# Kernel optimization log

Measured on AMD Instinct MI355X. Metric: run time of the kernel, lower is better.

The kernel has to match this reference:

```python
import jax, jax.numpy as jnp
import numpy as np

N = 50000       # num nodes
E = 800000      # num edges (before self loops)
D_IN = 128
D_H = 128
D_OUT = 40


def setup_inputs() -> dict:
    key = jax.random.key(0)
    ks = jax.random.split(key, 8)
    x = jax.random.normal(ks[0], (N, D_IN), dtype=jnp.float32)
    edge_index = jax.random.randint(ks[1], (2, E), 0, N, dtype=jnp.int32)
    # GCNConv weights (glorot-ish scale) and biases
    W1 = jax.random.normal(ks[2], (D_IN, D_H), dtype=jnp.float32) / np.sqrt(D_IN)
    b1 = jnp.zeros((D_H,), dtype=jnp.float32)
    W2 = jax.random.normal(ks[3], (D_H, D_H), dtype=jnp.float32) / np.sqrt(D_H)
    b2 = jnp.zeros((D_H,), dtype=jnp.float32)
    Wc = jax.random.normal(ks[4], (D_H, D_OUT), dtype=jnp.float32) / np.sqrt(D_H)
    bc = jnp.zeros((D_OUT,), dtype=jnp.float32)
    return {"x": x, "edge_index": edge_index, "W1": W1, "b1": b1,
            "W2": W2, "b2": b2, "Wc": Wc, "bc": bc}


def _gcn_conv(x, row, col, num_nodes, W, b):
    # PyG GCNConv: h = X @ W; out[c] += norm(r,c) * h[r]; out += b
    h = x @ W
    deg = jax.ops.segment_sum(jnp.ones(row.shape[0], h.dtype), col,
                              num_segments=num_nodes)
    dinv = jnp.where(deg > 0, jax.lax.rsqrt(deg), 0.0).astype(h.dtype)
    norm = dinv[row] * dinv[col]                      # [E+N]
    msg = h[row] * norm[:, None]                      # gather + scale
    agg = jax.ops.segment_sum(msg, col, num_segments=num_nodes)  # scatter-add
    return agg + b


def reference(x, edge_index, W1, b1, W2, b2, Wc, bc):
    # add self loops (GCNConv default add_self_loops=True)
    loops = jnp.arange(N, dtype=edge_index.dtype)
    row = jnp.concatenate([edge_index[0], loops])
    col = jnp.concatenate([edge_index[1], loops])
    h = jax.nn.relu(_gcn_conv(x, row, col, N, W1, b1))
    h = jax.nn.relu(_gcn_conv(h, row, col, N, W2, b2))
    g = jnp.mean(h, axis=0)                           # mean pool over nodes
    return g @ Wc + bc                                # [D_OUT]
```

## Files before the change

### kernel.cpp

```cpp
#include <hip/hip_runtime.h>
#include <hip/hip_fp16.h>


typedef _Float16 half8 __attribute__((ext_vector_type(8)));
typedef float f32x4 __attribute__((ext_vector_type(4)));
typedef float f32x2 __attribute__((ext_vector_type(2)));

constexpr int N = 50000;
constexpr int E = 800000;
constexpr int D = 128;
constexpr int DOUT = 40;
constexpr int CAP = 64;
constexpr int HB = 128;
constexpr int EPB = E / HB;
constexpr int HWRD = 12500;
constexpr int GM = (N + 127) / 128;
constexpr int NW = N / 4;
constexpr int GF = 3 * GM;

__global__ __launch_bounds__(1024) void k_hist(const int* __restrict__ col,
                                               unsigned char* __restrict__ hist,
                                               unsigned char* __restrict__ rank,
                                               const float* __restrict__ W1,
                                               const float* __restrict__ W2,
                                               __half* __restrict__ T1,
                                               __half* __restrict__ T2) {
    __shared__ unsigned int h[HWRD];
    int b = blockIdx.x, t = threadIdx.x;
    if (b >= HB) {
        int o = (b - HB) * 1024 + t;
        const float* W = (o < 16384) ? W1 : W2;
        __half* T = (o < 16384) ? T1 : T2;
        int oo = o & 16383;
        int n = oo >> 7, k = oo & 127;
        T[oo] = (__half)W[k * 128 + n];
        return;
    }
    for (int i = t; i < HWRD; i += 1024) h[i] = 0;
    __syncthreads();
    int e0 = b * EPB;
    for (int e = e0 + t; e < e0 + EPB; e += 1024) {
        int c = col[e];
        unsigned int old = atomicAdd(&h[c >> 2], 1u << ((c & 3) * 8));
        rank[e] = (unsigned char)((old >> ((c & 3) * 8)) & 0xff);
    }
    __syncthreads();
    unsigned int* out = (unsigned int*)(hist + (size_t)b * 50000);
    for (int i = t; i < HWRD; i += 1024) out[i] = h[i];
}

__global__ __launch_bounds__(256) void k_colscan(unsigned char* __restrict__ hist,
                                                 int* __restrict__ deg,
                                                 float* __restrict__ dinv) {
    __shared__ unsigned int part[4][64];
    unsigned int* hw = (unsigned int*)hist;
    int c4 = blockIdx.x * 64 + (threadIdx.x & 63);
    int qq = threadIdx.x >> 6;
    bool ok = c4 < HWRD;
    unsigned int v[32];
    unsigned int s = 0;
    if (ok) {
#pragma unroll
        for (int i = 0; i < 32; ++i) v[i] = hw[(size_t)(qq * 32 + i) * HWRD + c4];
#pragma unroll
        for (int i = 0; i < 32; ++i) s += v[i];
    }
    part[qq][threadIdx.x & 63] = s;
    __syncthreads();
    unsigned int base = 0;
    for (int k = 0; k < qq; ++k) base += part[k][threadIdx.x & 63];
    if (ok) {
        unsigned int run = base;
#pragma unroll
        for (int i = 0; i < 32; ++i) {
            hw[(size_t)(qq * 32 + i) * HWRD + c4] = run;
            run += v[i];
        }
        if (qq == 3) {
#pragma unroll
            for (int j = 0; j < 4; ++j) {
                int dg = (run >> (8 * j)) & 0xff;
                deg[4 * c4 + j] = dg;
                dinv[4 * c4 + j] = rsqrtf((float)(dg + 1));
            }
        }
    }
}

__device__ __forceinline__ unsigned char f8enc(float v) {
    return (unsigned char)(__builtin_amdgcn_cvt_pk_fp8_f32(v, v, 0, false) & 0xff);
}
__device__ __forceinline__ void add8f8(f32x2* a, uint2 u) {
    a[0] += __builtin_amdgcn_cvt_pk_f32_fp8(u.x, false);
    a[1] += __builtin_amdgcn_cvt_pk_f32_fp8(u.x, true);
    a[2] += __builtin_amdgcn_cvt_pk_f32_fp8(u.y, false);
    a[3] += __builtin_amdgcn_cvt_pk_f32_fp8(u.y, true);
}

__device__ __forceinline__ half8 ldA(const float* rowp, int koff) {
    float4 u0 = *(const float4*)(rowp + koff);
    float4 u1 = *(const float4*)(rowp + koff + 4);
    half8 r;
    r[0] = (_Float16)u0.x; r[1] = (_Float16)u0.y;
    r[2] = (_Float16)u0.z; r[3] = (_Float16)u0.w;
    r[4] = (_Float16)u1.x; r[5] = (_Float16)u1.y;
    r[6] = (_Float16)u1.z; r[7] = (_Float16)u1.w;
    return r;
}
__device__ __forceinline__ half8 ldA(const unsigned char* rowp, int koff) {
    uint2 u = *(const uint2*)(rowp + koff);
    f32x2 f0 = __builtin_amdgcn_cvt_pk_f32_fp8(u.x, false);
    f32x2 f1 = __builtin_amdgcn_cvt_pk_f32_fp8(u.x, true);
    f32x2 f2 = __builtin_amdgcn_cvt_pk_f32_fp8(u.y, false);
    f32x2 f3 = __builtin_amdgcn_cvt_pk_f32_fp8(u.y, true);
    half8 r;
    r[0] = (_Float16)f0[0]; r[1] = (_Float16)f0[1];
    r[2] = (_Float16)f1[0]; r[3] = (_Float16)f1[1];
    r[4] = (_Float16)f2[0]; r[5] = (_Float16)f2[1];
    r[6] = (_Float16)f3[0]; r[7] = (_Float16)f3[1];
    return r;
}

template <typename TA>
__device__ __forceinline__ void mfma_gemm(const TA* __restrict__ A,
                                          const __half* __restrict__ Wt,
                                          const float* __restrict__ dinv,
                                          unsigned char* __restrict__ out8,
                                          int row0, int tid) {
    int wave = tid >> 6, lane = tid & 63;
    int quad = lane >> 4, c16 = lane & 15;
    int m0 = row0 + wave * 32;
    int ra = m0 + c16;      if (ra >= N) ra = 0;
    int rb = m0 + 16 + c16; if (rb >= N) rb = 0;
    const TA* pa = A + (size_t)ra * D;
    const TA* pb = A + (size_t)rb * D;

    f32x4 acc[2][8];
#pragma unroll
    for (int i = 0; i < 2; ++i)
#pragma unroll
        for (int j = 0; j < 8; ++j) acc[i][j] = (f32x4){0.f, 0.f, 0.f, 0.f};

#pragma unroll
    for (int kq = 0; kq < 4; ++kq) {
        int koff = kq * 32 + quad * 8;
        half8 a0 = ldA(pa, koff);
        half8 a1 = ldA(pb, koff);
#pragma unroll
        for (int nt = 0; nt < 8; ++nt) {
            half8 bf = *(const half8*)(Wt + (size_t)(nt * 16 + c16) * D + koff);
            acc[0][nt] = __builtin_amdgcn_mfma_f32_16x16x32_f16(a0, bf, acc[0][nt], 0, 0, 0);
            acc[1][nt] = __builtin_amdgcn_mfma_f32_16x16x32_f16(a1, bf, acc[1][nt], 0, 0, 0);
        }
    }

#pragma unroll
    for (int rt = 0; rt < 2; ++rt) {
        int mt = m0 + rt * 16;
#pragma unroll
        for (int i = 0; i < 4; ++i) {
            int grow = mt + quad * 4 + i;
            if (grow < N) {
                float s = dinv[grow];
                unsigned char* orow = out8 + (size_t)grow * D + c16;
#pragma unroll
                for (int nt = 0; nt < 8; ++nt)
                    orow[nt * 16] = f8enc(acc[rt][nt][i] * s);
            }
        }
    }
}

__global__ __launch_bounds__(256) void k_fuse(const int* __restrict__ ei,
                                              const unsigned char* __restrict__ hist,
                                              const unsigned char* __restrict__ rank,
                                              unsigned short* __restrict__ csr,
                                              const float* __restrict__ x,
                                              const __half* __restrict__ Wt1,
                                              const float* __restrict__ dinv,
                                              unsigned char* __restrict__ out8) {
    int b = blockIdx.x, m = b % 3;
    if (m < 2) {
        int sb = (b / 3) * 2 + m;
        int e0 = sb * 1024 + threadIdx.x * 4;
        if (e0 >= E) return;
        int4 rr = *(const int4*)(ei + e0);
        int4 cc = *(const int4*)(ei + E + e0);
        uchar4 kk = *(const uchar4*)(rank + e0);
        int rs[4] = {rr.x, rr.y, rr.z, rr.w};
        int cs[4] = {cc.x, cc.y, cc.z, cc.w};
        int ks[4] = {kk.x, kk.y, kk.z, kk.w};
#pragma unroll
        for (int i = 0; i < 4; ++i) {
            int e = e0 + i;
            int c = cs[i];
            int chunk = e / EPB;
            int slot = (int)hist[(size_t)chunk * 50000 + c] + ks[i];
            if (slot < CAP) csr[(c << 6) + slot] = (unsigned short)rs[i];
        }
        return;
    }
    mfma_gemm<float>(x, Wt1, dinv, out8, (b / 3) * 128, threadIdx.x);
}

__device__ __forceinline__ float agg_core(int c, int lane,
                                          const unsigned char* __restrict__ hs8,
                                          const int* __restrict__ deg,
                                          const unsigned short* __restrict__ csr,
                                          float* __restrict__ a0out) {
    int qw = lane >> 4;
    int q  = lane & 15;
    int dgRaw = deg[c];
    int dg = dgRaw < CAP ? dgRaw : CAP;
    float dc = rsqrtf((float)(dgRaw + 1));
    int e0 = c << 6;

    f32x2 a0[4], a1[4], a2[4], a3[4];
#pragma unroll
    for (int i = 0; i < 4; ++i) {
        a0[i] = (f32x2){0.f, 0.f}; a1[i] = (f32x2){0.f, 0.f};
        a2[i] = (f32x2){0.f, 0.f}; a3[i] = (f32x2){0.f, 0.f};
    }
    if (qw == 0)
        add8f8(a0, *(const uint2*)&hs8[((unsigned)c << 7) + q * 8]);

    int j = 0;
    for (; j + 16 <= dg; j += 16) {
        int r0 = csr[e0 + j + qw];
        int r1 = csr[e0 + j + 4 + qw];
        int r2 = csr[e0 + j + 8 + qw];
        int r3 = csr[e0 + j + 12 + qw];
        uint2 u0 = *(const uint2*)&hs8[((unsigned)r0 << 7) + q * 8];
        uint2 u1 = *(const uint2*)&hs8[((unsigned)r1 << 7) + q * 8];
        uint2 u2 = *(const uint2*)&hs8[((unsigned)r2 << 7) + q * 8];
        uint2 u3 = *(const uint2*)&hs8[((unsigned)r3 << 7) + q * 8];
        add8f8(a0, u0); add8f8(a1, u1); add8f8(a2, u2); add8f8(a3, u3);
    }
    if (j + 8 <= dg) {
        int r0 = csr[e0 + j + qw];
        int r1 = csr[e0 + j + 4 + qw];
        uint2 u0 = *(const uint2*)&hs8[((unsigned)r0 << 7) + q * 8];
        uint2 u1 = *(const uint2*)&hs8[((unsigned)r1 << 7) + q * 8];
        add8f8(a0, u0); add8f8(a1, u1);
        j += 8;
    }
    if (j + 4 <= dg) {
        int r0 = csr[e0 + j + qw];
        add8f8(a0, *(const uint2*)&hs8[((unsigned)r0 << 7) + q * 8]);
        j += 4;
    }
    int rem = dg - j;
    if (qw < rem) {
        int r0 = csr[e0 + j + qw];
        add8f8(a1, *(const uint2*)&hs8[((unsigned)r0 << 7) + q * 8]);
    }

#pragma unroll
    for (int i = 0; i < 4; ++i) { a0[i] += a1[i]; a2[i] += a3[i]; a0[i] += a2[i]; }
#pragma unroll
    for (int t = 0; t < 8; ++t) {
        float v = a0[t >> 1][t & 1];
        v += __shfl_xor(v, 16, 64);
        v += __shfl_xor(v, 32, 64);
        a0out[t] = v;
    }
    return dc;
}

__global__ __launch_bounds__(256) void k_agg1(const unsigned char* __restrict__ hs8,
                                              const int* __restrict__ deg,
                                              const unsigned short* __restrict__ csr,
                                              const float* __restrict__ bias,
                                              unsigned char* __restrict__ out8) {
    int wave = threadIdx.x >> 6;
    int lane = threadIdx.x & 63;
    int c = blockIdx.x * 4 + wave;
    float a0[8];
    float dc = agg_core(c, lane, hs8, deg, csr, a0);
    if ((lane >> 4) == 0) {
        int q = lane & 15;
        union { unsigned char b[8]; uint2 u; } p;
#pragma unroll
        for (int i = 0; i < 8; ++i)
            p.b[i] = f8enc(fmaxf(fmaf(dc, a0[i], bias[q * 8 + i]), 0.f));
        *(uint2*)&out8[((unsigned)c << 7) + q * 8] = p.u;
    }
}

__global__ __launch_bounds__(256) void k_gemm(const unsigned char* __restrict__ A,
                                              const __half* __restrict__ Wt,
                                              const float* __restrict__ dinv,
                                              unsigned char* __restrict__ out8) {
    mfma_gemm<unsigned char>(A, Wt, dinv, out8, blockIdx.x * 128, threadIdx.x);
}

__global__ __launch_bounds__(256) void k_agg2(const unsigned char* __restrict__ hs8,
                                              const int* __restrict__ deg,
                                              const unsigned short* __restrict__ csr,
                                              const float* __restrict__ bias,
                                              float* __restrict__ gpart) {
    __shared__ float gblk[4][128];
    int wave = threadIdx.x >> 6;
    int lane = threadIdx.x & 63;
    int c = blockIdx.x * 4 + wave;
    float a0[8];
    float dc = agg_core(c, lane, hs8, deg, csr, a0);
    if ((lane >> 4) == 0) {
        int q = lane & 15;
#pragma unroll
        for (int i = 0; i < 8; ++i)
            gblk[wave][q * 8 + i] = fmaxf(fmaf(dc, a0[i], bias[q * 8 + i]), 0.f);
    }
    __syncthreads();
    int t = threadIdx.x;
    if (t < 128)
        gpart[(size_t)blockIdx.x * 128 + t] =
            gblk[0][t] + gblk[1][t] + gblk[2][t] + gblk[3][t];
}

__global__ __launch_bounds__(256) void k_pool(const float* __restrict__ gpart,
                                              float* __restrict__ gpart2) {
    int d = threadIdx.x & 127;
    int half = threadIdx.x >> 7;
    int b = blockIdx.x;
    int per = (NW + 255) / 256;
    int r0 = b * per;
    int r1 = r0 + per;
    if (r1 > NW) r1 = NW;
    float acc = 0.f;
    for (int r = r0 + half; r < r1; r += 2)
        acc += gpart[(size_t)r * D + d];
    __shared__ float red[256];
    red[threadIdx.x] = acc;
    __syncthreads();
    if (half == 0) gpart2[(size_t)b * D + d] = red[d] + red[128 + d];
}

__global__ __launch_bounds__(512) void k_final(const float* __restrict__ gpart2,
                                               const float* __restrict__ Wc,
                                               const float* __restrict__ bc,
                                               float* __restrict__ out) {
    __shared__ float g[D];
    __shared__ float red[512];
    int t = threadIdx.x;
    int d = t & 127, grp = t >> 7;
    float s = 0.f;
#pragma unroll 4
    for (int w = grp * 64; w < grp * 64 + 64; ++w)
        s += gpart2[(size_t)w * D + d];
    red[t] = s;
    __syncthreads();
    if (grp == 0)
        g[d] = (red[d] + red[128 + d] + red[256 + d] + red[384 + d]) * (1.0f / (float)N);
    __syncthreads();
    if (t < DOUT) {
        float acc = bc[t];
        for (int dd = 0; dd < D; ++dd) acc = fmaf(g[dd], Wc[dd * DOUT + t], acc);
        out[t] = acc;
    }
}

extern "C" void kernel_launch(void* const* d_in, const int* in_sizes, int n_in,
                              void* d_out, int out_size, void* d_ws, size_t ws_size,
                              hipStream_t stream) {
    const float* x  = (const float*)d_in[0];
    const int*   ei = (const int*)d_in[1];
    const float* W1 = (const float*)d_in[2];
    const float* b1 = (const float*)d_in[3];
    const float* W2 = (const float*)d_in[4];
    const float* b2 = (const float*)d_in[5];
    const float* Wc = (const float*)d_in[6];
    const float* bc = (const float*)d_in[7];
    float* out = (float*)d_out;

    char* ws = (char*)d_ws;
    size_t off = 0;
    auto alloc = [&](size_t bytes) {
        void* p = ws + off;
        off += (bytes + 511) & ~(size_t)511;
        return p;
    };
    unsigned char*  hist   = (unsigned char*) alloc((size_t)HB * 50000);
    unsigned char*  rank   = (unsigned char*) alloc((size_t)E);
    int*            deg    = (int*)           alloc((size_t)N * 4);
    float*          dinv   = (float*)         alloc((size_t)N * 4);
    unsigned short* csr    = (unsigned short*)alloc((size_t)N * CAP * 2);
    unsigned char*  hs8    = (unsigned char*) alloc((size_t)N * D);
    unsigned char*  h18    = (unsigned char*) alloc((size_t)N * D);
    __half*         Wt1    = (__half*)        alloc((size_t)D * D * 2);
    __half*         Wt2    = (__half*)        alloc((size_t)D * D * 2);
    float*          gpart  = (float*)         alloc((size_t)NW * D * 4);
    float*          gpart2 = (float*)         alloc((size_t)256 * D * 4);
    (void)ws_size; (void)in_sizes; (void)n_in; (void)out_size;

    const int* col = ei + E;

    k_hist<<<HB + 32, 1024, 0, stream>>>(col, hist, rank, W1, W2, Wt1, Wt2);
    k_colscan<<<(HWRD + 63) / 64, 256, 0, stream>>>(hist, deg, dinv);
    k_fuse<<<GF, 256, 0, stream>>>(ei, hist, rank, csr, x, Wt1, dinv, hs8);

    k_agg1<<<NW, 256, 0, stream>>>(hs8, deg, csr, b1, h18);
    k_gemm<<<GM, 256, 0, stream>>>(h18, Wt2, dinv, hs8);
    k_agg2<<<NW, 256, 0, stream>>>(hs8, deg, csr, b2, gpart);
    k_pool<<<256, 256, 0, stream>>>(gpart, gpart2);
    k_final<<<1, 512, 0, stream>>>(gpart2, Wc, bc, out);
}
```

Baseline: 206.3 us.

## Widen aggregation gathers to 16-byte rows and halve histogram block count

The neighbor aggregation now gives each source row to 8 lanes, each loading 16 bytes, so one wave covers 8 neighbors per step. All 64 CSR slots are read up front, and the feature loads are issued under per-slot predicates before any accumulation. This replaces the old variable-length loop and its tail handling, aiming for more loads in flight and fewer loop branches, at the cost of more registers. The edge histogram also drops from 128 to 64 chunks, which halves the histogram traffic and the column-scan work but gives each histogram block more edges to process.

Result: slower. 213.4 us (+3.5%).

```diff
diff --git a/kernel.cpp b/kernel.cpp
--- a/kernel.cpp
+++ b/kernel.cpp
@@ -11,7 +11,7 @@
 constexpr int D = 128;
 constexpr int DOUT = 40;
 constexpr int CAP = 64;
-constexpr int HB = 128;
+constexpr int HB = 64;
 constexpr int EPB = E / HB;
 constexpr int HWRD = 12500;
 constexpr int GM = (N + 127) / 128;
@@ -57,13 +57,13 @@
     int c4 = blockIdx.x * 64 + (threadIdx.x & 63);
     int qq = threadIdx.x >> 6;
     bool ok = c4 < HWRD;
-    unsigned int v[32];
+    unsigned int v[16];
     unsigned int s = 0;
     if (ok) {
 #pragma unroll
-        for (int i = 0; i < 32; ++i) v[i] = hw[(size_t)(qq * 32 + i) * HWRD + c4];
-#pragma unroll
-        for (int i = 0; i < 32; ++i) s += v[i];
+        for (int i = 0; i < 16; ++i) v[i] = hw[(size_t)(qq * 16 + i) * HWRD + c4];
+#pragma unroll
+        for (int i = 0; i < 16; ++i) s += v[i];
     }
     part[qq][threadIdx.x & 63] = s;
     __syncthreads();
@@ -72,8 +72,8 @@
     if (ok) {
         unsigned int run = base;
 #pragma unroll
-        for (int i = 0; i < 32; ++i) {
-            hw[(size_t)(qq * 32 + i) * HWRD + c4] = run;
+        for (int i = 0; i < 16; ++i) {
+            hw[(size_t)(qq * 16 + i) * HWRD + c4] = run;
             run += v[i];
         }
         if (qq == 3) {
@@ -90,11 +90,15 @@
 __device__ __forceinline__ unsigned char f8enc(float v) {
     return (unsigned char)(__builtin_amdgcn_cvt_pk_fp8_f32(v, v, 0, false) & 0xff);
 }
-__device__ __forceinline__ void add8f8(f32x2* a, uint2 u) {
+__device__ __forceinline__ void add16f8(f32x2* a, uint4 u) {
     a[0] += __builtin_amdgcn_cvt_pk_f32_fp8(u.x, false);
     a[1] += __builtin_amdgcn_cvt_pk_f32_fp8(u.x, true);
     a[2] += __builtin_amdgcn_cvt_pk_f32_fp8(u.y, false);
     a[3] += __builtin_amdgcn_cvt_pk_f32_fp8(u.y, true);
+    a[4] += __builtin_amdgcn_cvt_pk_f32_fp8(u.z, false);
+    a[5] += __builtin_amdgcn_cvt_pk_f32_fp8(u.z, true);
+    a[6] += __builtin_amdgcn_cvt_pk_f32_fp8(u.w, false);
+    a[7] += __builtin_amdgcn_cvt_pk_f32_fp8(u.w, true);
 }
 
 __device__ __forceinline__ half8 ldA(const float* rowp, int koff) {
@@ -208,58 +212,40 @@
                                           const int* __restrict__ deg,
                                           const unsigned short* __restrict__ csr,
                                           float* __restrict__ a0out) {
-    int qw = lane >> 4;
-    int q  = lane & 15;
+    int qw = lane >> 3;
+    int q  = lane & 7;
     int dgRaw = deg[c];
     int dg = dgRaw < CAP ? dgRaw : CAP;
     float dc = rsqrtf((float)(dgRaw + 1));
     int e0 = c << 6;
-
-    f32x2 a0[4], a1[4], a2[4], a3[4];
-#pragma unroll
-    for (int i = 0; i < 4; ++i) {
-        a0[i] = (f32x2){0.f, 0.f}; a1[i] = (f32x2){0.f, 0.f};
-        a2[i] = (f32x2){0.f, 0.f}; a3[i] = (f32x2){0.f, 0.f};
-    }
-    if (qw == 0)
-        add8f8(a0, *(const uint2*)&hs8[((unsigned)c << 7) + q * 8]);
-
-    int j = 0;
-    for (; j + 16 <= dg; j += 16) {
-        int r0 = csr[e0 + j + qw];
-        int r1 = csr[e0 + j + 4 + qw];
-        int r2 = csr[e0 + j + 8 + qw];
-        int r3 = csr[e0 + j + 12 + qw];
-        uint2 u0 = *(const uint2*)&hs8[((unsigned)r0 << 7) + q * 8];
-        uint2 u1 = *(const uint2*)&hs8[((unsigned)r1 << 7) + q * 8];
-        uint2 u2 = *(const uint2*)&hs8[((unsigned)r2 << 7) + q * 8];
-        uint2 u3 = *(const uint2*)&hs8[((unsigned)r3 << 7) + q * 8];
-        add8f8(a0, u0); add8f8(a1, u1); add8f8(a2, u2); add8f8(a3, u3);
-    }
-    if (j + 8 <= dg) {
-        int r0 = csr[e0 + j + qw];
-        int r1 = csr[e0 + j + 4 + qw];
-        uint2 u0 = *(const uint2*)&hs8[((unsigned)r0 << 7) + q * 8];
-        uint2 u1 = *(const uint2*)&hs8[((unsigned)r1 << 7) + q * 8];
-        add8f8(a0, u0); add8f8(a1, u1);
-        j += 8;
-    }
-    if (j + 4 <= dg) {
-        int r0 = csr[e0 + j + qw];
-        add8f8(a0, *(const uint2*)&hs8[((unsigned)r0 << 7) + q * 8]);
-        j += 4;
-    }
-    int rem = dg - j;
-    if (qw < rem) {
-        int r0 = csr[e0 + j + qw];
-        add8f8(a1, *(const uint2*)&hs8[((unsigned)r0 << 7) + q * 8]);
-    }
-
-#pragma unroll
-    for (int i = 0; i < 4; ++i) { a0[i] += a1[i]; a2[i] += a3[i]; a0[i] += a2[i]; }
-#pragma unroll
-    for (int t = 0; t < 8; ++t) {
-        float v = a0[t >> 1][t & 1];
+    int boff = q * 16;
+
+    int r[8];
+#pragma unroll
+    for (int b = 0; b < 8; ++b) r[b] = csr[e0 + b * 8 + qw];
+
+    uint4 us;
+    bool selfv = (qw == 0);
+    if (selfv) us = *(const uint4*)&hs8[((unsigned)c << 7) + boff];
+
+    uint4 u[8];
+#pragma unroll
+    for (int b = 0; b < 8; ++b)
+        if (b * 8 + qw < dg)
+            u[b] = *(const uint4*)&hs8[((unsigned)r[b] << 7) + boff];
+
+    f32x2 acc[8];
+#pragma unroll
+    for (int i = 0; i < 8; ++i) acc[i] = (f32x2){0.f, 0.f};
+    if (selfv) add16f8(acc, us);
+#pragma unroll
+    for (int b = 0; b < 8; ++b)
+        if (b * 8 + qw < dg) add16f8(acc, u[b]);
+
+#pragma unroll
+    for (int t = 0; t < 16; ++t) {
+        float v = acc[t >> 1][t & 1];
+        v += __shfl_xor(v, 8, 64);
         v += __shfl_xor(v, 16, 64);
         v += __shfl_xor(v, 32, 64);
         a0out[t] = v;
@@ -275,15 +261,15 @@
     int wave = threadIdx.x >> 6;
     int lane = threadIdx.x & 63;
     int c = blockIdx.x * 4 + wave;
-    float a0[8];
+    float a0[16];
     float dc = agg_core(c, lane, hs8, deg, csr, a0);
-    if ((lane >> 4) == 0) {
-        int q = lane & 15;
-        union { unsigned char b[8]; uint2 u; } p;
-#pragma unroll
-        for (int i = 0; i < 8; ++i)
-            p.b[i] = f8enc(fmaxf(fmaf(dc, a0[i], bias[q * 8 + i]), 0.f));
-        *(uint2*)&out8[((unsigned)c << 7) + q * 8] = p.u;
+    if (lane < 8) {
+        int q = lane;
+        union { unsigned char b[16]; uint4 u; } p;
+#pragma unroll
+        for (int i = 0; i < 16; ++i)
+            p.b[i] = f8enc(fmaxf(fmaf(dc, a0[i], bias[q * 16 + i]), 0.f));
+        *(uint4*)&out8[((unsigned)c << 7) + q * 16] = p.u;
     }
 }
 
@@ -303,13 +289,13 @@
     int wave = threadIdx.x >> 6;
     int lane = threadIdx.x & 63;
     int c = blockIdx.x * 4 + wave;
-    float a0[8];
+    float a0[16];
     float dc = agg_core(c, lane, hs8, deg, csr, a0);
-    if ((lane >> 4) == 0) {
-        int q = lane & 15;
-#pragma unroll
-        for (int i = 0; i < 8; ++i)
-            gblk[wave][q * 8 + i] = fmaxf(fmaf(dc, a0[i], bias[q * 8 + i]), 0.f);
+    if (lane < 8) {
+        int q = lane;
+#pragma unroll
+        for (int i = 0; i < 16; ++i)
+            gblk[wave][q * 16 + i] = fmaxf(fmaf(dc, a0[i], bias[q * 16 + i]), 0.f);
     }
     __syncthreads();
     int t = threadIdx.x;
```

## Reorder layer-2 as aggregate-then-GEMM and fuse bias/ReLU/mean-pool into GEMM epilogue

Applied to the files above, without the earlier changes.

Layer 2 now aggregates first, over dinv-prescaled layer-1 activations (A·h·W = (A·h)·W), and runs the GEMM afterwards. Bias, ReLU and column sums go into the GEMM epilogue, so the per-node partial buffer and the separate pool kernel are no longer needed. This removes one kernel launch and the large gpart write/read pass. In exchange the aggregation input is quantized to fp8 after scaling by dinv and again after aggregation, which may change precision.

After: 209.4 us. About the same (+1.5%).

```diff
diff --git a/kernel.cpp b/kernel.cpp
--- a/kernel.cpp
+++ b/kernel.cpp
@@ -121,19 +121,18 @@
     return r;
 }
 
-template <typename TA>
-__device__ __forceinline__ void mfma_gemm(const TA* __restrict__ A,
-                                          const __half* __restrict__ Wt,
-                                          const float* __restrict__ dinv,
-                                          unsigned char* __restrict__ out8,
-                                          int row0, int tid) {
+__device__ __forceinline__ void mfma_gemm1(const float* __restrict__ A,
+                                           const __half* __restrict__ Wt,
+                                           const float* __restrict__ dinv,
+                                           unsigned char* __restrict__ out8,
+                                           int row0, int tid) {
     int wave = tid >> 6, lane = tid & 63;
     int quad = lane >> 4, c16 = lane & 15;
     int m0 = row0 + wave * 32;
     int ra = m0 + c16;      if (ra >= N) ra = 0;
     int rb = m0 + 16 + c16; if (rb >= N) rb = 0;
-    const TA* pa = A + (size_t)ra * D;
-    const TA* pb = A + (size_t)rb * D;
+    const float* pa = A + (size_t)ra * D;
+    const float* pb = A + (size_t)rb * D;
 
     f32x4 acc[2][8];
 #pragma unroll
@@ -200,7 +199,7 @@
         }
         return;
     }
-    mfma_gemm<float>(x, Wt1, dinv, out8, (b / 3) * 128, threadIdx.x);
+    mfma_gemm1(x, Wt1, dinv, out8, (b / 3) * 128, threadIdx.x);
 }
 
 __device__ __forceinline__ float agg_core(int c, int lane,
@@ -271,6 +270,7 @@
                                               const int* __restrict__ deg,
                                               const unsigned short* __restrict__ csr,
                                               const float* __restrict__ bias,
+                                              const float* __restrict__ dinv,
                                               unsigned char* __restrict__ out8) {
     int wave = threadIdx.x >> 6;
     int lane = threadIdx.x & 63;
@@ -279,64 +279,90 @@
     float dc = agg_core(c, lane, hs8, deg, csr, a0);
     if ((lane >> 4) == 0) {
         int q = lane & 15;
+        float sc = dinv[c];
         union { unsigned char b[8]; uint2 u; } p;
 #pragma unroll
         for (int i = 0; i < 8; ++i)
-            p.b[i] = f8enc(fmaxf(fmaf(dc, a0[i], bias[q * 8 + i]), 0.f));
+            p.b[i] = f8enc(sc * fmaxf(fmaf(dc, a0[i], bias[q * 8 + i]), 0.f));
         *(uint2*)&out8[((unsigned)c << 7) + q * 8] = p.u;
     }
 }
 
-__global__ __launch_bounds__(256) void k_gemm(const unsigned char* __restrict__ A,
-                                              const __half* __restrict__ Wt,
-                                              const float* __restrict__ dinv,
-                                              unsigned char* __restrict__ out8) {
-    mfma_gemm<unsigned char>(A, Wt, dinv, out8, blockIdx.x * 128, threadIdx.x);
-}
-
-__global__ __launch_bounds__(256) void k_agg2(const unsigned char* __restrict__ hs8,
-                                              const int* __restrict__ deg,
-                                              const unsigned short* __restrict__ csr,
-                                              const float* __restrict__ bias,
-                                              float* __restrict__ gpart) {
-    __shared__ float gblk[4][128];
+__global__ __launch_bounds__(256) void k_agg2p(const unsigned char* __restrict__ s1,
+                                               const int* __restrict__ deg,
+                                               const unsigned short* __restrict__ csr,
+                                               unsigned char* __restrict__ outA) {
     int wave = threadIdx.x >> 6;
     int lane = threadIdx.x & 63;
     int c = blockIdx.x * 4 + wave;
     float a0[8];
-    float dc = agg_core(c, lane, hs8, deg, csr, a0);
+    float dc = agg_core(c, lane, s1, deg, csr, a0);
     if ((lane >> 4) == 0) {
         int q = lane & 15;
+        union { unsigned char b[8]; uint2 u; } p;
 #pragma unroll
         for (int i = 0; i < 8; ++i)
-            gblk[wave][q * 8 + i] = fmaxf(fmaf(dc, a0[i], bias[q * 8 + i]), 0.f);
-    }
-    __syncthreads();
-    int t = threadIdx.x;
-    if (t < 128)
-        gpart[(size_t)blockIdx.x * 128 + t] =
-            gblk[0][t] + gblk[1][t] + gblk[2][t] + gblk[3][t];
-}
-
-__global__ __launch_bounds__(256) void k_pool(const float* __restrict__ gpart,
-                                              float* __restrict__ gpart2) {
-    int d = threadIdx.x & 127;
-    int half = threadIdx.x >> 7;
-    int b = blockIdx.x;
-    int per = (NW + 255) / 256;
-    int r0 = b * per;
-    int r1 = r0 + per;
-    if (r1 > NW) r1 = NW;
-    float acc = 0.f;
-    for (int r = r0 + half; r < r1; r += 2)
-        acc += gpart[(size_t)r * D + d];
-    __shared__ float red[256];
-    red[threadIdx.x] = acc;
-    __syncthreads();
-    if (half == 0) gpart2[(size_t)b * D + d] = red[d] + red[128 + d];
-}
-
-__global__ __launch_bounds__(512) void k_final(const float* __restrict__ gpart2,
+            p.b[i] = f8enc(dc * a0[i]);
+        *(uint2*)&outA[((unsigned)c << 7) + q * 8] = p.u;
+    }
+}
+
+__global__ __launch_bounds__(256) void k_gemmpool(const unsigned char* __restrict__ A,
+                                                  const __half* __restrict__ Wt,
+                                                  const float* __restrict__ bias,
+                                                  float* __restrict__ gpart) {
+    __shared__ float colsum[4][128];
+    int tid = threadIdx.x;
+    int wave = tid >> 6, lane = tid & 63;
+    int quad = lane >> 4, c16 = lane & 15;
+    int m0 = blockIdx.x * 128 + wave * 32;
+    int ra = m0 + c16;      if (ra >= N) ra = 0;
+    int rb = m0 + 16 + c16; if (rb >= N) rb = 0;
+    const unsigned char* pa = A + (size_t)ra * D;
+    const unsigned char* pb = A + (size_t)rb * D;
+
+    f32x4 acc[2][8];
+#pragma unroll
+    for (int i = 0; i < 2; ++i)
+#pragma unroll
+        for (int j = 0; j < 8; ++j) acc[i][j] = (f32x4){0.f, 0.f, 0.f, 0.f};
+
+#pragma unroll
+    for (int kq = 0; kq < 4; ++kq) {
+        int koff = kq * 32 + quad * 8;
+        half8 a0 = ldA(pa, koff);
+        half8 a1 = ldA(pb, koff);
+#pragma unroll
+        for (int nt = 0; nt < 8; ++nt) {
+            half8 bf = *(const half8*)(Wt + (size_t)(nt * 16 + c16) * D + koff);
+            acc[0][nt] = __builtin_amdgcn_mfma_f32_16x16x32_f16(a0, bf, acc[0][nt], 0, 0, 0);
+            acc[1][nt] = __builtin_amdgcn_mfma_f32_16x16x32_f16(a1, bf, acc[1][nt], 0, 0, 0);
+        }
+    }
+
+#pragma unroll
+    for (int nt = 0; nt < 8; ++nt) {
+        float bv = bias[nt * 16 + c16];
+        float s = 0.f;
+#pragma unroll
+        for (int rt = 0; rt < 2; ++rt) {
+#pragma unroll
+            for (int i = 0; i < 4; ++i) {
+                int grow = m0 + rt * 16 + quad * 4 + i;
+                if (grow < N) s += fmaxf(acc[rt][nt][i] + bv, 0.f);
+            }
+        }
+        s += __shfl_xor(s, 16, 64);
+        s += __shfl_xor(s, 32, 64);
+        if (quad == 0) colsum[wave][nt * 16 + c16] = s;
+    }
+    __syncthreads();
+    if (tid < 128)
+        gpart[(size_t)blockIdx.x * 128 + tid] =
+            colsum[0][tid] + colsum[1][tid] + colsum[2][tid] + colsum[3][tid];
+}
+
+__global__ __launch_bounds__(512) void k_final(const float* __restrict__ gpart,
                                                const float* __restrict__ Wc,
                                                const float* __restrict__ bc,
                                                float* __restrict__ out) {
@@ -345,9 +371,8 @@
     int t = threadIdx.x;
     int d = t & 127, grp = t >> 7;
     float s = 0.f;
-#pragma unroll 4
-    for (int w = grp * 64; w < grp * 64 + 64; ++w)
-        s += gpart2[(size_t)w * D + d];
+    for (int w = grp; w < GM; w += 4)
+        s += gpart[(size_t)w * D + d];
     red[t] = s;
     __syncthreads();
     if (grp == 0)
@@ -386,11 +411,11 @@
     float*          dinv   = (float*)         alloc((size_t)N * 4);
     unsigned short* csr    = (unsigned short*)alloc((size_t)N * CAP * 2);
     unsigned char*  hs8    = (unsigned char*) alloc((size_t)N * D);
-    unsigned char*  h18    = (unsigned char*) alloc((size_t)N * D);
+    unsigned char*  s18    = (unsigned char*) alloc((size_t)N * D);
+    unsigned char*  aact   = (unsigned char*) alloc((size_t)N * D);
     __half*         Wt1    = (__half*)        alloc((size_t)D * D * 2);
     __half*         Wt2    = (__half*)        alloc((size_t)D * D * 2);
-    float*          gpart  = (float*)         alloc((size_t)NW * D * 4);
-    float*          gpart2 = (float*)         alloc((size_t)256 * D * 4);
+    float*          gpart  = (float*)         alloc((size_t)GM * D * 4);
     (void)ws_size; (void)in_sizes; (void)n_in; (void)out_size;
 
     const int* col = ei + E;
@@ -399,9 +424,8 @@
     k_colscan<<<(HWRD + 63) / 64, 256, 0, stream>>>(hist, deg, dinv);
     k_fuse<<<GF, 256, 0, stream>>>(ei, hist, rank, csr, x, Wt1, dinv, hs8);
 
-    k_agg1<<<NW, 256, 0, stream>>>(hs8, deg, csr, b1, h18);
-    k_gemm<<<GM, 256, 0, stream>>>(h18, Wt2, dinv, hs8);
-    k_agg2<<<NW, 256, 0, stream>>>(hs8, deg, csr, b2, gpart);
-    k_pool<<<256, 256, 0, stream>>>(gpart, gpart2);
-    k_final<<<1, 512, 0, stream>>>(gpart2, Wc, bc, out);
-}
+    k_agg1<<<NW, 256, 0, stream>>>(hs8, deg, csr, b1, dinv, s18);
+    k_agg2p<<<NW, 256, 0, stream>>>(s18, deg, csr, aact);
+    k_gemmpool<<<GM, 256, 0, stream>>>(aact, Wt2, b2, gpart);
+    k_final<<<1, 512, 0, stream>>>(gpart, Wc, bc, out);
+}
```
